# Optimization experiments

Hardware: AMD Instinct MI355X
Metric: run time of the kernel (lower is better)

The kernel has to match this reference:

```python
import jax, jax.numpy as jnp
import numpy as np

B, C, NQ, NK, S, H, FF = 8, 256, 1024, 4096, 16, 8, 2048
DH = C // H
EPS = 1e-5


def _layernorm(x, g, b):
    m = jnp.mean(x, axis=-1, keepdims=True)
    v = jnp.mean((x - m) ** 2, axis=-1, keepdims=True)
    return (x - m) * jax.lax.rsqrt(v + EPS) * g + b


def _box_query(key_pos, query_pos):
    # key_pos: (B,NK,3); query_pos: (B,NQ,6) = centers ++ box sizes (L,H,W)
    centers = query_pos[:, :, None, :3]            # (B,NQ,1,3)
    half = 0.5 * query_pos[:, :, None, 3:]         # (B,NQ,1,3)
    off = jnp.abs(key_pos[:, None, :, :] - centers)  # (B,NQ,NK,3)
    inside = jnp.all(off <= half, axis=-1)         # (B,NQ,NK)
    # first n_sample inside-points in index order (stable sort: inside first)
    order = jnp.argsort(~inside, axis=-1, stable=True)
    idx = order[..., :S]                           # (B,NQ,S)
    valid = jnp.take_along_axis(inside, idx, axis=-1)
    mask = ~valid                                  # True = padded / masked
    idx = jnp.where(mask, 0, idx)
    mask = mask.at[..., 0].set(False)              # matches cuda path: slot 0 never masked
    return idx, mask


def _forward(query, key, query_pos, key_pos,
             q_w, q_b, k_w, k_b, v_w, v_b, o_w, o_b,
             lin1_w, lin1_b, lin2_w, lin2_b,
             n1_g, n1_b, n2_g, n2_b, qpe_w, qpe_b, kpe_w, kpe_b):
    idx, mask = _box_query(key_pos, query_pos)     # (B,NQ,S), (B,NQ,S)
    # gather neighborhoods
    gxyz = jax.vmap(lambda kp, ix: kp[ix])(key_pos, idx)        # (B,NQ,S,3)
    gxyz = gxyz - query_pos[:, :, None, :3]                     # center-relative
    gfeat = jax.vmap(lambda kf, ix: kf[:, ix])(key, idx)        # (B,C,NQ,S)

    BQ = B * NQ
    kfeat = jnp.transpose(gfeat, (0, 2, 3, 1)).reshape(BQ, S, C)   # (BQ,S,C)
    kpe = gxyz.reshape(BQ, S, 3) @ kpe_w.T + kpe_b                 # cross_embed
    qtok = jnp.transpose(query, (0, 2, 1)).reshape(BQ, C)          # (BQ,C)
    qpe = (query_pos @ qpe_w.T + qpe_b).reshape(BQ, C)             # pos_embed

    # multihead cross-attention: 1 query vs S=16 local keys per group
    kv_in = kfeat + kpe
    qh = ((qtok + qpe) @ q_w.T + q_b).reshape(BQ, H, DH)
    kh = (kv_in @ k_w.T + k_b).reshape(BQ, S, H, DH)
    vh = (kv_in @ v_w.T + v_b).reshape(BQ, S, H, DH)
    scores = jnp.einsum('bhd,bshd->bhs', qh, kh) / np.sqrt(DH)    # (BQ,H,S)
    scores = jnp.where(mask.reshape(BQ, 1, S), -1e30, scores)
    attn = jax.nn.softmax(scores, axis=-1)
    ao = jnp.einsum('bhs,bshd->bhd', attn, vh).reshape(BQ, C)
    ao = ao @ o_w.T + o_b

    x = _layernorm(qtok + ao, n1_g, n1_b)                         # post-norm
    ff = jax.nn.relu(x @ lin1_w.T + lin1_b) @ lin2_w.T + lin2_b
    x = _layernorm(x + ff, n2_g, n2_b)
    return jnp.transpose(x.reshape(B, NQ, C), (0, 2, 1))          # (B,C,NQ)


def setup_inputs() -> dict:
    rng = jax.random.key(0)
    ks = jax.random.split(rng, 24)
    s = 0.02
    query = jax.random.normal(ks[0], (B, C, NQ), jnp.float32)
    key = jax.random.normal(ks[1], (B, C, NK), jnp.float32)
    key_pos = jax.random.uniform(ks[2], (B, NK, 3), jnp.float32)
    centers = jax.random.uniform(ks[3], (B, NQ, 3), jnp.float32)
    sizes = jax.random.uniform(ks[4], (B, NQ, 3), jnp.float32, minval=0.1, maxval=0.4)
    query_pos = jnp.concatenate([centers, sizes], axis=-1)
    p = {
        'q_w': jax.random.normal(ks[5], (C, C)) * s, 'q_b': jnp.zeros((C,)),
        'k_w': jax.random.normal(ks[6], (C, C)) * s, 'k_b': jnp.zeros((C,)),
        'v_w': jax.random.normal(ks[7], (C, C)) * s, 'v_b': jnp.zeros((C,)),
        'o_w': jax.random.normal(ks[8], (C, C)) * s, 'o_b': jnp.zeros((C,)),
        'lin1_w': jax.random.normal(ks[9], (FF, C)) * s, 'lin1_b': jnp.zeros((FF,)),
        'lin2_w': jax.random.normal(ks[10], (C, FF)) * s, 'lin2_b': jnp.zeros((C,)),
        'n1_g': jnp.ones((C,)), 'n1_b': jnp.zeros((C,)),
        'n2_g': jnp.ones((C,)), 'n2_b': jnp.zeros((C,)),
        'qpe_w': jax.random.normal(ks[11], (C, 6)) * s, 'qpe_b': jnp.zeros((C,)),
        'kpe_w': jax.random.normal(ks[12], (C, 3)) * s, 'kpe_b': jnp.zeros((C,)),
    }
    return dict(query=query, key=key, query_pos=query_pos, key_pos=key_pos, **p)


def reference(query, key, query_pos, key_pos,
              q_w, q_b, k_w, k_b, v_w, v_b, o_w, o_b,
              lin1_w, lin1_b, lin2_w, lin2_b,
              n1_g, n1_b, n2_g, n2_b, qpe_w, qpe_b, kpe_w, kpe_b):
    return _forward(query, key, query_pos, key_pos,
                    q_w, q_b, k_w, k_b, v_w, v_b, o_w, o_b,
                    lin1_w, lin1_b, lin2_w, lin2_b,
                    n1_g, n1_b, n2_g, n2_b, qpe_w, qpe_b, kpe_w, kpe_b)
```

## Files before the change

### kernel.cpp

```cpp
#include <hip/hip_runtime.h>
#include <cstdint>

#define B_   8
#define C_   256
#define NQ_  1024
#define NK_  4096
#define S_   16
#define H_   8
#define FF_  2048
#define DH_  32
#define BQ_  (B_*NQ_)
#define EPS_ 1e-5f
#define KS_  8

typedef __bf16 bf16x8 __attribute__((ext_vector_type(8)));
typedef __bf16 bf16x4 __attribute__((ext_vector_type(4)));
typedef float  f32x4  __attribute__((ext_vector_type(4)));

struct CvtArgs {
  const float* src[6];
  __bf16* dst[6];
};

__device__ __forceinline__ void gload_lds16(const void* g, void* l) {
  __builtin_amdgcn_global_load_lds(
      (const __attribute__((address_space(1))) void*)g,
      (__attribute__((address_space(3))) void*)l, 16, 0, 0);
}

#define SEGA 2048
#define SEGB 10240
#define SEGC 12288
#define SEGD 13568
#define NPREP 13584

__global__ __launch_bounds__(256) void k_prep(
    const float* __restrict__ query, const float* __restrict__ key,
    const float* __restrict__ query_pos, const float* __restrict__ key_pos,
    const float* __restrict__ qpe_w, const float* __restrict__ qpe_b,
    const float* __restrict__ k_w, const float* __restrict__ k_b,
    const float* __restrict__ v_w, const float* __restrict__ v_b,
    const float* __restrict__ kpe_w, const float* __restrict__ kpe_b,
    CvtArgs ca,
    __bf16* __restrict__ keyTb, __bf16* __restrict__ qtokb,
    __bf16* __restrict__ qinb,
    float4* __restrict__ Pk, float4* __restrict__ Pv,
    int* __restrict__ idxo, int* __restrict__ masko) {
  __shared__ __align__(16) float smem[1248];
  int blk = blockIdx.x, t = threadIdx.x;
  int tx = t & 31, ty = t >> 5;

  if (blk < SEGA) {
    int lane = t & 63;
    int q = blk * 4 + (t >> 6);
    int b = q >> 10;
    const float* kpb = key_pos + (size_t)b * NK_ * 3;
    const float* qp = query_pos + (size_t)q * 6;
    float cx = qp[0], cy = qp[1], cz = qp[2];
    float hx = 0.5f * qp[3], hy = 0.5f * qp[4], hz = 0.5f * qp[5];
    int* iq = idxo + (size_t)q * S_;
    int found = 0;
    for (int ch = 0; ch < NK_ / 64; ch += 4) {
      float dx[4], dy[4], dz[4];
#pragma unroll
      for (int u = 0; u < 4; ++u) {
        int k = (ch + u) * 64 + lane;
        dx[u] = fabsf(kpb[k * 3 + 0] - cx);
        dy[u] = fabsf(kpb[k * 3 + 1] - cy);
        dz[u] = fabsf(kpb[k * 3 + 2] - cz);
      }
#pragma unroll
      for (int u = 0; u < 4; ++u) {
        bool inside = (dx[u] <= hx) && (dy[u] <= hy) && (dz[u] <= hz);
        unsigned long long bal = __ballot(inside);
        if (inside) {
          int slot = found + __popcll(bal & ((1ull << lane) - 1ull));
          if (slot < S_) iq[slot] = (ch + u) * 64 + lane;
        }
        found += __popcll(bal);
      }
      if (found >= S_) break;
    }
    if (found > S_) found = S_;
    if (lane < S_) {
      int m = (lane < found) ? 0 : 1;
      if (lane >= found) iq[lane] = 0;
      if (lane == 0) m = 0;
      masko[(size_t)q * S_ + lane] = m;
    }
  } else if (blk < SEGB) {
    int local = blk - SEGA;
    float (*tt)[33] = (float(*)[33])smem;
    int x = local & 127, y = (local >> 7) & 7, z = local >> 10;
    int j0 = x * 32, i0 = y * 32;
    const float* inz = key + (size_t)z * C_ * NK_;
    __bf16* outz = keyTb + (size_t)z * NK_ * C_;
#pragma unroll
    for (int r = 0; r < 32; r += 8)
      tt[ty + r][tx] = inz[(size_t)(i0 + ty + r) * NK_ + (j0 + tx)];
    __syncthreads();
#pragma unroll
    for (int r = 0; r < 32; r += 8)
      outz[(size_t)(j0 + ty + r) * C_ + (i0 + tx)] = (__bf16)tt[tx][ty + r];
  } else if (blk < SEGC) {
    int local = blk - SEGB;
    float (*tt)[33] = (float(*)[33])smem;
    float (*sqp)[6] = (float(*)[6])(smem + 1056);
    int x = local & 31, y = (local >> 5) & 7, z = local >> 8;
    int nq0 = x * 32, c0 = y * 32;
    const float* inz = query + (size_t)z * C_ * NQ_;
#pragma unroll
    for (int r = 0; r < 32; r += 8)
      tt[ty + r][tx] = inz[(size_t)(c0 + ty + r) * NQ_ + (nq0 + tx)];
    if (t < 192)
      sqp[t / 6][t % 6] = query_pos[((size_t)z * NQ_ + nq0 + t / 6) * 6 + (t % 6)];
    int c = c0 + tx;
    float w0 = qpe_w[c * 6 + 0], w1 = qpe_w[c * 6 + 1], w2 = qpe_w[c * 6 + 2];
    float w3 = qpe_w[c * 6 + 3], w4 = qpe_w[c * 6 + 4], w5 = qpe_w[c * 6 + 5];
    float wb = qpe_b[c];
    __syncthreads();
#pragma unroll
    for (int r = 0; r < 32; r += 8) {
      int nql = ty + r;
      size_t row = (size_t)z * NQ_ + nq0 + nql;
      float v = tt[tx][nql];
      float pe = wb + sqp[nql][0] * w0 + sqp[nql][1] * w1 + sqp[nql][2] * w2 +
                 sqp[nql][3] * w3 + sqp[nql][4] * w4 + sqp[nql][5] * w5;
      qtokb[row * C_ + c] = (__bf16)v;
      qinb[row * C_ + c] = (__bf16)(v + pe);
    }
  } else if (blk < SEGD) {
    int local = blk - SEGC;
    int idx, base;
    if (local < 64)       { idx = 0; base = local; }
    else if (local < 128) { idx = 1; base = local - 64; }
    else if (local < 192) { idx = 2; base = local - 128; }
    else if (local < 256) { idx = 3; base = local - 192; }
    else if (local < 768) { idx = 4; base = local - 256; }
    else                  { idx = 5; base = local - 768; }
    size_t off = (size_t)base * 1024 + t * 4;
    float4 v = *(const float4*)(ca.src[idx] + off);
    __bf16* o = ca.dst[idx] + off;
    o[0] = (__bf16)v.x; o[1] = (__bf16)v.y; o[2] = (__bf16)v.z; o[3] = (__bf16)v.w;
  } else {
    int local = blk - SEGD;
    int bx = local & 7, bv = local >> 3;
    const float* w  = bv ? v_w : k_w;
    const float* wb = bv ? v_b : k_b;
    float4* P = bv ? Pv : Pk;
    float4 (*red)[8] = (float4(*)[8])smem;
    int nl = t >> 3, ks = (t & 7) * 32;
    int n = bx * 32 + nl;
    const float* wr = w + (size_t)n * C_;
    float p0 = 0.f, p1 = 0.f, p2 = 0.f, pb = 0.f;
#pragma unroll
    for (int k = ks; k < ks + 32; ++k) {
      float wv = wr[k];
      p0 += kpe_w[k * 3 + 0] * wv;
      p1 += kpe_w[k * 3 + 1] * wv;
      p2 += kpe_w[k * 3 + 2] * wv;
      pb += kpe_b[k] * wv;
    }
    red[nl][t & 7] = make_float4(p0, p1, p2, pb);
    __syncthreads();
    if (t < 32) {
      float4 s = red[t][0];
#pragma unroll
      for (int j = 1; j < 8; ++j) {
        float4 r = red[t][j];
        s.x += r.x; s.y += r.y; s.z += r.z; s.w += r.w;
      }
      s.w += wb[bx * 32 + t];
      P[bx * 32 + t] = s;
    }
  }
}

template <int BM, int BN, int RELU, int OUT_BF16>
__device__ __forceinline__ void gemm_body(
    const __bf16* __restrict__ A, const __bf16* __restrict__ Wn,
    const float* __restrict__ bias, void* __restrict__ outp,
    int n0, int m0, int N, int K, int kbeg, int kend) {
  constexpr int MI = BM / 32, JN = BN / 32;
  constexpr int AI = BM / 32, BI = BN / 32;
  __shared__ __align__(16) __bf16 As[BM][64];
  __shared__ __align__(16) __bf16 Bs[BN][64];
  int t = threadIdx.x;
  int lane = t & 63, w = t >> 6;
  int lane16 = lane & 15, quad = lane >> 4;
  int wm = (w & 1) * (BM / 2), wn = (w >> 1) * (BN / 2);
  int l3 = lane >> 3;
  int lc = lane & 7;

  f32x4 acc[MI][JN];
#pragma unroll
  for (int i = 0; i < MI; ++i)
#pragma unroll
    for (int j = 0; j < JN; ++j) acc[i][j] = (f32x4){0.f, 0.f, 0.f, 0.f};

  for (int k0 = kbeg; k0 < kend; k0 += 64) {
#pragma unroll
    for (int i = 0; i < AI; ++i) {
      int j = i * 4 + w;
      int row = j * 8 + l3;
      const __bf16* src = A + (size_t)(m0 + row) * K + k0 + ((lc ^ l3) << 3);
      gload_lds16(src, (char*)&As[0][0] + j * 1024);
    }
#pragma unroll
    for (int i = 0; i < BI; ++i) {
      int j = i * 4 + w;
      int row = j * 8 + l3;
      const __bf16* src = Wn + (size_t)(n0 + row) * K + k0 + ((lc ^ l3) << 3);
      gload_lds16(src, (char*)&Bs[0][0] + j * 1024);
    }
    __syncthreads();
#pragma unroll
    for (int kk = 0; kk < 64; kk += 32) {
      bf16x8 af[MI], bfr[JN];
      int qc = (kk >> 3) + quad;
#pragma unroll
      for (int i = 0; i < MI; ++i) {
        int row = wm + i * 16 + lane16;
        int ch = qc ^ (lane16 & 7);
        af[i] = *(const bf16x8*)((const char*)&As[row][0] + ch * 16);
      }
#pragma unroll
      for (int j = 0; j < JN; ++j) {
        int row = wn + j * 16 + lane16;
        int ch = qc ^ (lane16 & 7);
        bfr[j] = *(const bf16x8*)((const char*)&Bs[row][0] + ch * 16);
      }
#pragma unroll
      for (int i = 0; i < MI; ++i)
#pragma unroll
        for (int j = 0; j < JN; ++j)
          acc[i][j] = __builtin_amdgcn_mfma_f32_16x16x32_bf16(af[i], bfr[j], acc[i][j], 0, 0, 0);
    }
    __syncthreads();
  }

#pragma unroll
  for (int j = 0; j < JN; ++j) {
    int col = n0 + wn + j * 16 + lane16;
    float bv = bias ? bias[col] : 0.f;
#pragma unroll
    for (int i = 0; i < MI; ++i) {
#pragma unroll
      for (int r = 0; r < 4; ++r) {
        int row = m0 + wm + i * 16 + quad * 4 + r;
        float v = acc[i][j][r] + bv;
        if (RELU) v = fmaxf(v, 0.f);
        if (OUT_BF16)
          ((__bf16*)outp)[(size_t)row * N + col] = (__bf16)v;
        else
          ((float*)outp)[(size_t)row * N + col] = v;
      }
    }
  }
}

template <int BM, int BN, int RELU, int OUT_BF16>
__global__ __launch_bounds__(256) void k_gemm(
    const __bf16* __restrict__ A, const __bf16* __restrict__ Wn,
    const float* __restrict__ bias, void* __restrict__ outp, int N, int K) {
  gemm_body<BM, BN, RELU, OUT_BF16>(A, Wn, bias, outp,
                                    blockIdx.x * BN, blockIdx.y * BM, N, K, 0, K);
}

__global__ __launch_bounds__(256) void k_gemmsk(
    const __bf16* __restrict__ A, const __bf16* __restrict__ Wn,
    __bf16* __restrict__ partials) {
  int ks = blockIdx.z;
  int kbeg = ks * (FF_ / KS_), kend = kbeg + FF_ / KS_;
  gemm_body<128, 128, 0, 1>(A, Wn, nullptr,
                            partials + (size_t)ks * BQ_ * C_,
                            blockIdx.x * 128, blockIdx.y * 128, C_, FF_, kbeg, kend);
}

__global__ __launch_bounds__(256) void k_gemmsko(
    const __bf16* __restrict__ A, const __bf16* __restrict__ Wn,
    __bf16* __restrict__ partials) {
  int ks = blockIdx.z;
  int kbeg = ks * 128, kend = kbeg + 128;
  gemm_body<128, 64, 0, 1>(A, Wn, nullptr,
                           partials + (size_t)ks * BQ_ * C_,
                           blockIdx.x * 64, blockIdx.y * 128, C_, C_, kbeg, kend);
}

__global__ __launch_bounds__(256) void k_gemm2(
    const __bf16* __restrict__ keyTb, const __bf16* __restrict__ kvwb,
    __bf16* __restrict__ khvbuf,
    const __bf16* __restrict__ qinb, const __bf16* __restrict__ qwb,
    const float* __restrict__ q_b, __bf16* __restrict__ qhb) {
  int blk = blockIdx.x;
  const __bf16 *A, *Wn; const float* bias; __bf16* outp; int n0, m0, N;
  if (blk < 1024) {
    A = keyTb; Wn = kvwb; bias = nullptr; outp = khvbuf;
    n0 = (blk & 3) * 128; m0 = (blk >> 2) * 128; N = 512;
  } else {
    int l = blk - 1024;
    A = qinb; Wn = qwb; bias = q_b; outp = qhb;
    n0 = (l & 1) * 128; m0 = (l >> 1) * 128; N = 256;
  }
  gemm_body<128, 128, 0, 1>(A, Wn, bias, outp, n0, m0, N, 256, 0, 256);
}

__global__ __launch_bounds__(256) void k_attnf(
    const __bf16* __restrict__ khv,
    const float* __restrict__ key_pos,
    const float* __restrict__ query_pos,
    const int* __restrict__ idx,
    const int* __restrict__ maskb,
    const __bf16* __restrict__ qhb,
    const float4* __restrict__ Pk,
    const float4* __restrict__ Pv,
    __bf16* __restrict__ aob) {
  __shared__ __bf16 kvs[S_][520];
  __shared__ float qrow[C_];
  __shared__ float sc[H_][S_];
  __shared__ float pw[H_][S_];
  __shared__ float4 gx4[S_];
  __shared__ float4 pgxs[H_];
  __shared__ float4 qpks[H_];
  __shared__ int srow[S_], smask[S_];
  int bq = blockIdx.x, b = bq >> 10, t = threadIdx.x;

  if (t < S_) {
    int k = idx[(size_t)bq * S_ + t];
    srow[t] = b * NK_ + k;
    smask[t] = maskb[(size_t)bq * S_ + t];
    const float* kpp = key_pos + ((size_t)b * NK_ + k) * 3;
    const float* qp  = query_pos + (size_t)bq * 6;
    gx4[t] = make_float4(kpp[0] - qp[0], kpp[1] - qp[1], kpp[2] - qp[2], 1.f);
  }
  float qv_t = (float)qhb[(size_t)bq * C_ + t];
  qrow[t] = qv_t;
  {
    float4 p = Pk[t];
    p.x *= qv_t; p.y *= qv_t; p.z *= qv_t; p.w *= qv_t;
#pragma unroll
    for (int off = 16; off >= 1; off >>= 1) {
      p.x += __shfl_xor(p.x, off);
      p.y += __shfl_xor(p.y, off);
      p.z += __shfl_xor(p.z, off);
      p.w += __shfl_xor(p.w, off);
    }
    if ((t & 31) == 0) {
      const float s = 0.17677669529663687f;
      qpks[t >> 5] = make_float4(p.x * s, p.y * s, p.z * s, p.w * s);
    }
  }
  __syncthreads();
  {
    int s = t >> 4, c0 = (t & 15) * 32;
    const __bf16* src = khv + (size_t)srow[s] * 512 + c0;
    *(bf16x8*)&kvs[s][c0]      = *(const bf16x8*)&src[0];
    *(bf16x8*)&kvs[s][c0 + 8]  = *(const bf16x8*)&src[8];
    *(bf16x8*)&kvs[s][c0 + 16] = *(const bf16x8*)&src[16];
    *(bf16x8*)&kvs[s][c0 + 24] = *(const bf16x8*)&src[24];
  }
  __syncthreads();
  if (t < H_ * S_) {
    int h = t >> 4, s = t & (S_ - 1);
    float d = 0.f;
#pragma unroll
    for (int c0 = 0; c0 < 32; c0 += 8) {
      bf16x8 xv = *(const bf16x8*)&kvs[s][h * 32 + c0];
#pragma unroll
      for (int j = 0; j < 8; ++j) d += qrow[h * 32 + c0 + j] * (float)xv[j];
    }
    d *= 0.17677669529663687f;
    float4 g = gx4[s];
    float4 pk = qpks[h];
    d += g.x * pk.x + g.y * pk.y + g.z * pk.z + pk.w;
    if (smask[s]) d = -1e30f;
    sc[h][s] = d;
  }
  __syncthreads();
  if (t < H_) {
    float mx = -3.4e38f;
#pragma unroll
    for (int s = 0; s < S_; ++s) mx = fmaxf(mx, sc[t][s]);
    float e[S_], sum = 0.f;
#pragma unroll
    for (int s = 0; s < S_; ++s) { e[s] = expf(sc[t][s] - mx); sum += e[s]; }
    float inv = 1.f / sum;
    float gxx = 0.f, gyy = 0.f, gzz = 0.f;
#pragma unroll
    for (int s = 0; s < S_; ++s) {
      float p = e[s] * inv;
      pw[t][s] = p;
      float4 g = gx4[s];
      gxx += p * g.x; gyy += p * g.y; gzz += p * g.z;
    }
    pgxs[t] = make_float4(gxx, gyy, gzz, 1.f);
  }
  __syncthreads();
  {
    int h = t >> 5;
    float a = 0.f;
#pragma unroll
    for (int s = 0; s < S_; ++s) a += pw[h][s] * (float)kvs[s][256 + t];
    float4 pv = Pv[t];
    float4 g = pgxs[h];
    a += g.x * pv.x + g.y * pv.y + g.z * pv.z + pv.w;
    aob[(size_t)bq * C_ + t] = (__bf16)a;
  }
}

__global__ __launch_bounds__(256) void k_ln1(const __bf16* __restrict__ xa,
                                             const __bf16* __restrict__ op2,
                                             const float* __restrict__ obias,
                                             const float* __restrict__ g,
                                             const float* __restrict__ bb,
                                             __bf16* __restrict__ outb) {
  int wid = (blockIdx.x * 256 + threadIdx.x) >> 6;
  int lane = threadIdx.x & 63;
  bf16x4 va = *(const bf16x4*)&xa[(size_t)wid * C_ + lane * 4];
  float4 ob4 = *(const float4*)(obias + lane * 4);
  bf16x4 p0 = *(const bf16x4*)&op2[(size_t)wid * C_ + lane * 4];
  bf16x4 p1 = *(const bf16x4*)&op2[(size_t)BQ_ * C_ + (size_t)wid * C_ + lane * 4];
  float x0 = (float)va[0] + ob4.x + (float)p0[0] + (float)p1[0];
  float x1 = (float)va[1] + ob4.y + (float)p0[1] + (float)p1[1];
  float x2 = (float)va[2] + ob4.z + (float)p0[2] + (float)p1[2];
  float x3 = (float)va[3] + ob4.w + (float)p0[3] + (float)p1[3];
  float s = x0 + x1 + x2 + x3;
#pragma unroll
  for (int off = 32; off >= 1; off >>= 1) s += __shfl_xor(s, off);
  float mean = s * (1.f / C_);
  float d0 = x0 - mean, d1 = x1 - mean, d2 = x2 - mean, d3 = x3 - mean;
  float v = d0 * d0 + d1 * d1 + d2 * d2 + d3 * d3;
#pragma unroll
  for (int off = 32; off >= 1; off >>= 1) v += __shfl_xor(v, off);
  float inv = 1.f / sqrtf(v * (1.f / C_) + EPS_);
  float4 g4 = *(const float4*)(g + lane * 4);
  float4 b4 = *(const float4*)(bb + lane * 4);
  __bf16* obp = outb + (size_t)wid * C_ + lane * 4;
  obp[0] = (__bf16)(d0 * inv * g4.x + b4.x);
  obp[1] = (__bf16)(d1 * inv * g4.y + b4.y);
  obp[2] = (__bf16)(d2 * inv * g4.z + b4.z);
  obp[3] = (__bf16)(d3 * inv * g4.w + b4.w);
}

__global__ __launch_bounds__(256) void k_lnt(const __bf16* __restrict__ x1b,
                                             const __bf16* __restrict__ ff2p,
                                             const float* __restrict__ l2bias,
                                             const float* __restrict__ g,
                                             const float* __restrict__ bb,
                                             float* __restrict__ out) {
  __shared__ float buf[32][257];
  int z = blockIdx.y, nq0 = blockIdx.x * 32;
  int t = threadIdx.x;
  int w = t >> 6, lane = t & 63;
  float4 g4 = *(const float4*)(g + lane * 4);
  float4 b4 = *(const float4*)(bb + lane * 4);
  float4 l2b = *(const float4*)(l2bias + lane * 4);
#pragma unroll
  for (int rr = 0; rr < 8; ++rr) {
    int row = w * 8 + rr;
    size_t grow = (size_t)z * NQ_ + nq0 + row;
    bf16x4 va = *(const bf16x4*)&x1b[grow * C_ + lane * 4];
    float x0 = (float)va[0] + l2b.x, x1 = (float)va[1] + l2b.y;
    float x2 = (float)va[2] + l2b.z, x3 = (float)va[3] + l2b.w;
#pragma unroll
    for (int ks = 0; ks < KS_; ++ks) {
      bf16x4 p = *(const bf16x4*)&ff2p[((size_t)ks * BQ_ + grow) * C_ + lane * 4];
      x0 += (float)p[0]; x1 += (float)p[1]; x2 += (float)p[2]; x3 += (float)p[3];
    }
    float s = x0 + x1 + x2 + x3;
#pragma unroll
    for (int off = 32; off >= 1; off >>= 1) s += __shfl_xor(s, off);
    float mean = s * (1.f / C_);
    float d0 = x0 - mean, d1 = x1 - mean, d2 = x2 - mean, d3 = x3 - mean;
    float v = d0 * d0 + d1 * d1 + d2 * d2 + d3 * d3;
#pragma unroll
    for (int off = 32; off >= 1; off >>= 1) v += __shfl_xor(v, off);
    float inv = 1.f / sqrtf(v * (1.f / C_) + EPS_);
    buf[row][lane * 4 + 0] = d0 * inv * g4.x + b4.x;
    buf[row][lane * 4 + 1] = d1 * inv * g4.y + b4.y;
    buf[row][lane * 4 + 2] = d2 * inv * g4.z + b4.z;
    buf[row][lane * 4 + 3] = d3 * inv * g4.w + b4.w;
  }
  __syncthreads();
  int tx = t & 31, ty = t >> 5;
#pragma unroll
  for (int ci = 0; ci < 32; ++ci) {
    int c = ci * 8 + ty;
    out[((size_t)z * C_ + c) * NQ_ + nq0 + tx] = buf[tx][c];
  }
}

extern "C" void kernel_launch(void* const* d_in, const int* in_sizes, int n_in,
                              void* d_out, int out_size, void* d_ws, size_t ws_size,
                              hipStream_t stream) {
  const float* query     = (const float*)d_in[0];
  const float* key       = (const float*)d_in[1];
  const float* query_pos = (const float*)d_in[2];
  const float* key_pos   = (const float*)d_in[3];
  const float* q_w = (const float*)d_in[4];  const float* q_b = (const float*)d_in[5];
  const float* k_w = (const float*)d_in[6];  const float* k_b = (const float*)d_in[7];
  const float* v_w = (const float*)d_in[8];  const float* v_b = (const float*)d_in[9];
  const float* o_w = (const float*)d_in[10]; const float* o_b = (const float*)d_in[11];
  const float* lin1_w = (const float*)d_in[12]; const float* lin1_b = (const float*)d_in[13];
  const float* lin2_w = (const float*)d_in[14]; const float* lin2_b = (const float*)d_in[15];
  const float* n1_g = (const float*)d_in[16]; const float* n1_b = (const float*)d_in[17];
  const float* n2_g = (const float*)d_in[18]; const float* n2_b = (const float*)d_in[19];
  const float* qpe_w = (const float*)d_in[20]; const float* qpe_b = (const float*)d_in[21];
  const float* kpe_w = (const float*)d_in[22]; const float* kpe_b = (const float*)d_in[23];
  float* out = (float*)d_out;

  const size_t BQc = (size_t)BQ_ * C_;
  float* w = (float*)d_ws;
  size_t o = 0;
  __bf16* keyTb = (__bf16*)(w + o); o += (size_t)B_ * NK_ * C_ / 2;
  __bf16* qtokb = (__bf16*)(w + o); o += BQc / 2;
  __bf16* op2  = (__bf16*)(w + o); o += BQc;
  __bf16* khvbuf = (__bf16*)(w + o); o += (size_t)B_ * NK_ * 512 / 2;
  __bf16* ff2p = (__bf16*)(w + o); o += BQc * KS_ / 2;
  __bf16* qinb = (__bf16*)(w + o); o += BQc / 2;
  __bf16* qhb  = (__bf16*)(w + o); o += BQc / 2;
  __bf16* aob  = (__bf16*)(w + o); o += BQc / 2;
  __bf16* x1b  = (__bf16*)(w + o); o += BQc / 2;
  __bf16* qwb  = (__bf16*)(w + o); o += (size_t)C_ * C_ / 2;
  __bf16* kvwb = (__bf16*)(w + o); o += (size_t)C_ * C_;
  __bf16* owb  = (__bf16*)(w + o); o += (size_t)C_ * C_ / 2;
  __bf16* l1b  = (__bf16*)(w + o); o += (size_t)C_ * FF_ / 2;
  __bf16* l2b  = (__bf16*)(w + o); o += (size_t)C_ * FF_ / 2;
  float4* Pk   = (float4*)(w + o); o += C_ * 4;
  float4* Pv   = (float4*)(w + o); o += C_ * 4;
  int* idxb  = (int*)(w + o); o += (size_t)BQ_ * S_;
  int* maskb = (int*)(w + o); o += (size_t)BQ_ * S_;
  __bf16* ff1b = khvbuf;

  CvtArgs ca;
  ca.src[0] = q_w; ca.dst[0] = qwb;
  ca.src[1] = k_w; ca.dst[1] = kvwb;
  ca.src[2] = v_w; ca.dst[2] = kvwb + (size_t)C_ * C_;
  ca.src[3] = o_w; ca.dst[3] = owb;
  ca.src[4] = lin1_w; ca.dst[4] = l1b;
  ca.src[5] = lin2_w; ca.dst[5] = l2b;
  k_prep<<<NPREP, 256, 0, stream>>>(query, key, query_pos, key_pos,
                                    qpe_w, qpe_b, k_w, k_b, v_w, v_b,
                                    kpe_w, kpe_b, ca,
                                    keyTb, qtokb, qinb, Pk, Pv, idxb, maskb);
  k_gemm2<<<1024 + 128, 256, 0, stream>>>(keyTb, kvwb, khvbuf, qinb, qwb, q_b, qhb);
  k_attnf<<<BQ_, 256, 0, stream>>>(khvbuf, key_pos, query_pos, idxb, maskb,
                                   qhb, Pk, Pv, aob);
  k_gemmsko<<<dim3(C_ / 64, BQ_ / 128, 2), 256, 0, stream>>>(aob, owb, op2);
  k_ln1<<<BQ_ / 4, 256, 0, stream>>>(qtokb, op2, o_b, n1_g, n1_b, x1b);
  k_gemm<128, 128, 1, 1><<<dim3(FF_ / 128, BQ_ / 128), 256, 0, stream>>>(
      x1b, l1b, lin1_b, ff1b, FF_, C_);
  k_gemmsk<<<dim3(C_ / 128, BQ_ / 128, KS_), 256, 0, stream>>>(ff1b, l2b, ff2p);
  k_lnt<<<dim3(NQ_ / 32, B_), 256, 0, stream>>>(x1b, ff2p, lin2_b, n2_g, n2_b, out);
}
```

Measured before the change: 258.5 us.

## Widen GEMM tiles to 128x256, halve lin2 split-K, drop out-proj split-K

Result: slower. 277.7 us (+7.4%).

```diff
diff --git a/kernel.cpp b/kernel.cpp
--- a/kernel.cpp
+++ b/kernel.cpp
@@ -11,7 +11,7 @@
 #define DH_  32
 #define BQ_  (B_*NQ_)
 #define EPS_ 1e-5f
-#define KS_  8
+#define KS_  4
 
 typedef __bf16 bf16x8 __attribute__((ext_vector_type(8)));
 typedef __bf16 bf16x4 __attribute__((ext_vector_type(4)));
@@ -272,19 +272,9 @@
     __bf16* __restrict__ partials) {
   int ks = blockIdx.z;
   int kbeg = ks * (FF_ / KS_), kend = kbeg + FF_ / KS_;
-  gemm_body<128, 128, 0, 1>(A, Wn, nullptr,
+  gemm_body<128, 256, 0, 1>(A, Wn, nullptr,
                             partials + (size_t)ks * BQ_ * C_,
-                            blockIdx.x * 128, blockIdx.y * 128, C_, FF_, kbeg, kend);
-}
-
-__global__ __launch_bounds__(256) void k_gemmsko(
-    const __bf16* __restrict__ A, const __bf16* __restrict__ Wn,
-    __bf16* __restrict__ partials) {
-  int ks = blockIdx.z;
-  int kbeg = ks * 128, kend = kbeg + 128;
-  gemm_body<128, 64, 0, 1>(A, Wn, nullptr,
-                           partials + (size_t)ks * BQ_ * C_,
-                           blockIdx.x * 64, blockIdx.y * 128, C_, C_, kbeg, kend);
+                            blockIdx.x * 256, blockIdx.y * 128, C_, FF_, kbeg, kend);
 }
 
 __global__ __launch_bounds__(256) void k_gemm2(
@@ -294,15 +284,15 @@
     const float* __restrict__ q_b, __bf16* __restrict__ qhb) {
   int blk = blockIdx.x;
   const __bf16 *A, *Wn; const float* bias; __bf16* outp; int n0, m0, N;
-  if (blk < 1024) {
+  if (blk < 512) {
     A = keyTb; Wn = kvwb; bias = nullptr; outp = khvbuf;
-    n0 = (blk & 3) * 128; m0 = (blk >> 2) * 128; N = 512;
+    n0 = (blk & 1) * 256; m0 = (blk >> 1) * 128; N = 512;
   } else {
-    int l = blk - 1024;
+    int l = blk - 512;
     A = qinb; Wn = qwb; bias = q_b; outp = qhb;
-    n0 = (l & 1) * 128; m0 = (l >> 1) * 128; N = 256;
-  }
-  gemm_body<128, 128, 0, 1>(A, Wn, bias, outp, n0, m0, N, 256, 0, 256);
+    n0 = 0; m0 = l * 128; N = 256;
+  }
+  gemm_body<128, 256, 0, 1>(A, Wn, bias, outp, n0, m0, N, 256, 0, 256);
 }
 
 __global__ __launch_bounds__(256) void k_attnf(
@@ -409,21 +399,18 @@
 }
 
 __global__ __launch_bounds__(256) void k_ln1(const __bf16* __restrict__ xa,
-                                             const __bf16* __restrict__ op2,
-                                             const float* __restrict__ obias,
+                                             const __bf16* __restrict__ op,
                                              const float* __restrict__ g,
                                              const float* __restrict__ bb,
                                              __bf16* __restrict__ outb) {
   int wid = (blockIdx.x * 256 + threadIdx.x) >> 6;
   int lane = threadIdx.x & 63;
   bf16x4 va = *(const bf16x4*)&xa[(size_t)wid * C_ + lane * 4];
-  float4 ob4 = *(const float4*)(obias + lane * 4);
-  bf16x4 p0 = *(const bf16x4*)&op2[(size_t)wid * C_ + lane * 4];
-  bf16x4 p1 = *(const bf16x4*)&op2[(size_t)BQ_ * C_ + (size_t)wid * C_ + lane * 4];
-  float x0 = (float)va[0] + ob4.x + (float)p0[0] + (float)p1[0];
-  float x1 = (float)va[1] + ob4.y + (float)p0[1] + (float)p1[1];
-  float x2 = (float)va[2] + ob4.z + (float)p0[2] + (float)p1[2];
-  float x3 = (float)va[3] + ob4.w + (float)p0[3] + (float)p1[3];
+  bf16x4 p0 = *(const bf16x4*)&op[(size_t)wid * C_ + lane * 4];
+  float x0 = (float)va[0] + (float)p0[0];
+  float x1 = (float)va[1] + (float)p0[1];
+  float x2 = (float)va[2] + (float)p0[2];
+  float x3 = (float)va[3] + (float)p0[3];
   float s = x0 + x1 + x2 + x3;
 #pragma unroll
   for (int off = 32; off >= 1; off >>= 1) s += __shfl_xor(s, off);
@@ -514,7 +501,7 @@
   size_t o = 0;
   __bf16* keyTb = (__bf16*)(w + o); o += (size_t)B_ * NK_ * C_ / 2;
   __bf16* qtokb = (__bf16*)(w + o); o += BQc / 2;
-  __bf16* op2  = (__bf16*)(w + o); o += BQc;
+  __bf16* op   = (__bf16*)(w + o); o += BQc / 2;
   __bf16* khvbuf = (__bf16*)(w + o); o += (size_t)B_ * NK_ * 512 / 2;
   __bf16* ff2p = (__bf16*)(w + o); o += BQc * KS_ / 2;
   __bf16* qinb = (__bf16*)(w + o); o += BQc / 2;
@@ -543,13 +530,14 @@
                                     qpe_w, qpe_b, k_w, k_b, v_w, v_b,
                                     kpe_w, kpe_b, ca,
                                     keyTb, qtokb, qinb, Pk, Pv, idxb, maskb);
-  k_gemm2<<<1024 + 128, 256, 0, stream>>>(keyTb, kvwb, khvbuf, qinb, qwb, q_b, qhb);
+  k_gemm2<<<512 + 64, 256, 0, stream>>>(keyTb, kvwb, khvbuf, qinb, qwb, q_b, qhb);
   k_attnf<<<BQ_, 256, 0, stream>>>(khvbuf, key_pos, query_pos, idxb, maskb,
                                    qhb, Pk, Pv, aob);
-  k_gemmsko<<<dim3(C_ / 64, BQ_ / 128, 2), 256, 0, stream>>>(aob, owb, op2);
-  k_ln1<<<BQ_ / 4, 256, 0, stream>>>(qtokb, op2, o_b, n1_g, n1_b, x1b);
-  k_gemm<128, 128, 1, 1><<<dim3(FF_ / 128, BQ_ / 128), 256, 0, stream>>>(
+  k_gemm<128, 64, 0, 1><<<dim3(C_ / 64, BQ_ / 128), 256, 0, stream>>>(
+      aob, owb, o_b, op, C_, C_);
+  k_ln1<<<BQ_ / 4, 256, 0, stream>>>(qtokb, op, n1_g, n1_b, x1b);
+  k_gemm<128, 256, 1, 1><<<dim3(FF_ / 256, BQ_ / 128), 256, 0, stream>>>(
       x1b, l1b, lin1_b, ff1b, FF_, C_);
-  k_gemmsk<<<dim3(C_ / 128, BQ_ / 128, KS_), 256, 0, stream>>>(ff1b, l2b, ff2p);
+  k_gemmsk<<<dim3(1, BQ_ / 128, KS_), 256, 0, stream>>>(ff1b, l2b, ff2p);
   k_lnt<<<dim3(NQ_ / 32, B_), 256, 0, stream>>>(x1b, ff2p, lin2_b, n2_g, n2_b, out);
 }
```

## Fuse output-proj and FF2 GEMMs with layernorm epilogues, dropping split-K partials

Applied to the files above, without the earlier changes.

Measured after the change: 258.4 us. No clear change (-0.0%).

```diff
diff --git a/kernel.cpp b/kernel.cpp
--- a/kernel.cpp
+++ b/kernel.cpp
@@ -11,7 +11,6 @@
 #define DH_  32
 #define BQ_  (B_*NQ_)
 #define EPS_ 1e-5f
-#define KS_  8
 
 typedef __bf16 bf16x8 __attribute__((ext_vector_type(8)));
 typedef __bf16 bf16x4 __attribute__((ext_vector_type(4)));
@@ -176,21 +175,75 @@
   }
 }
 
+template <int BM, int BN>
+__device__ __forceinline__ void gemm_tile(
+    const __bf16* __restrict__ A, const __bf16* __restrict__ Wn,
+    int m0, int n0, int K, int kbeg, int kend,
+    __bf16 (*As)[64], __bf16 (*Bs)[64],
+    f32x4 (&acc)[BM / 32][BN / 32]) {
+  constexpr int MI = BM / 32, JN = BN / 32;
+  constexpr int AI = BM / 32, BI = BN / 32;
+  int t = threadIdx.x;
+  int lane = t & 63, w = t >> 6;
+  int lane16 = lane & 15, quad = lane >> 4;
+  int wm = (w & 1) * (BM / 2), wn = (w >> 1) * (BN / 2);
+  int l3 = lane >> 3;
+  int lc = lane & 7;
+
+  for (int k0 = kbeg; k0 < kend; k0 += 64) {
+#pragma unroll
+    for (int i = 0; i < AI; ++i) {
+      int j = i * 4 + w;
+      int row = j * 8 + l3;
+      const __bf16* src = A + (size_t)(m0 + row) * K + k0 + ((lc ^ l3) << 3);
+      gload_lds16(src, (char*)&As[0][0] + j * 1024);
+    }
+#pragma unroll
+    for (int i = 0; i < BI; ++i) {
+      int j = i * 4 + w;
+      int row = j * 8 + l3;
+      const __bf16* src = Wn + (size_t)(n0 + row) * K + k0 + ((lc ^ l3) << 3);
+      gload_lds16(src, (char*)&Bs[0][0] + j * 1024);
+    }
+    __syncthreads();
+#pragma unroll
+    for (int kk = 0; kk < 64; kk += 32) {
+      bf16x8 af[MI], bfr[JN];
+      int qc = (kk >> 3) + quad;
+#pragma unroll
+      for (int i = 0; i < MI; ++i) {
+        int row = wm + i * 16 + lane16;
+        int ch = qc ^ (lane16 & 7);
+        af[i] = *(const bf16x8*)((const char*)&As[row][0] + ch * 16);
+      }
+#pragma unroll
+      for (int j = 0; j < JN; ++j) {
+        int row = wn + j * 16 + lane16;
+        int ch = qc ^ (lane16 & 7);
+        bfr[j] = *(const bf16x8*)((const char*)&Bs[row][0] + ch * 16);
+      }
+#pragma unroll
+      for (int i = 0; i < MI; ++i)
+#pragma unroll
+        for (int j = 0; j < JN; ++j)
+          acc[i][j] = __builtin_amdgcn_mfma_f32_16x16x32_bf16(af[i], bfr[j], acc[i][j], 0, 0, 0);
+    }
+    __syncthreads();
+  }
+}
+
 template <int BM, int BN, int RELU, int OUT_BF16>
 __device__ __forceinline__ void gemm_body(
     const __bf16* __restrict__ A, const __bf16* __restrict__ Wn,
     const float* __restrict__ bias, void* __restrict__ outp,
     int n0, int m0, int N, int K, int kbeg, int kend) {
   constexpr int MI = BM / 32, JN = BN / 32;
-  constexpr int AI = BM / 32, BI = BN / 32;
   __shared__ __align__(16) __bf16 As[BM][64];
   __shared__ __align__(16) __bf16 Bs[BN][64];
   int t = threadIdx.x;
   int lane = t & 63, w = t >> 6;
   int lane16 = lane & 15, quad = lane >> 4;
   int wm = (w & 1) * (BM / 2), wn = (w >> 1) * (BN / 2);
-  int l3 = lane >> 3;
-  int lc = lane & 7;
 
   f32x4 acc[MI][JN];
 #pragma unroll
@@ -198,46 +251,7 @@
 #pragma unroll
     for (int j = 0; j < JN; ++j) acc[i][j] = (f32x4){0.f, 0.f, 0.f, 0.f};
 
-  for (int k0 = kbeg; k0 < kend; k0 += 64) {
-#pragma unroll
-    for (int i = 0; i < AI; ++i) {
-      int j = i * 4 + w;
-      int row = j * 8 + l3;
-      const __bf16* src = A + (size_t)(m0 + row) * K + k0 + ((lc ^ l3) << 3);
-      gload_lds16(src, (char*)&As[0][0] + j * 1024);
-    }
-#pragma unroll
-    for (int i = 0; i < BI; ++i) {
-      int j = i * 4 + w;
-      int row = j * 8 + l3;
-      const __bf16* src = Wn + (size_t)(n0 + row) * K + k0 + ((lc ^ l3) << 3);
-      gload_lds16(src, (char*)&Bs[0][0] + j * 1024);
-    }
-    __syncthreads();
-#pragma unroll
-    for (int kk = 0; kk < 64; kk += 32) {
-      bf16x8 af[MI], bfr[JN];
-      int qc = (kk >> 3) + quad;
-#pragma unroll
-      for (int i = 0; i < MI; ++i) {
-        int row = wm + i * 16 + lane16;
-        int ch = qc ^ (lane16 & 7);
-        af[i] = *(const bf16x8*)((const char*)&As[row][0] + ch * 16);
-      }
-#pragma unroll
-      for (int j = 0; j < JN; ++j) {
-        int row = wn + j * 16 + lane16;
-        int ch = qc ^ (lane16 & 7);
-        bfr[j] = *(const bf16x8*)((const char*)&Bs[row][0] + ch * 16);
-      }
-#pragma unroll
-      for (int i = 0; i < MI; ++i)
-#pragma unroll
-        for (int j = 0; j < JN; ++j)
-          acc[i][j] = __builtin_amdgcn_mfma_f32_16x16x32_bf16(af[i], bfr[j], acc[i][j], 0, 0, 0);
-    }
-    __syncthreads();
-  }
+  gemm_tile<BM, BN>(A, Wn, m0, n0, K, kbeg, kend, As, Bs, acc);
 
 #pragma unroll
   for (int j = 0; j < JN; ++j) {
@@ -265,26 +279,6 @@
     const float* __restrict__ bias, void* __restrict__ outp, int N, int K) {
   gemm_body<BM, BN, RELU, OUT_BF16>(A, Wn, bias, outp,
                                     blockIdx.x * BN, blockIdx.y * BM, N, K, 0, K);
-}
-
-__global__ __launch_bounds__(256) void k_gemmsk(
-    const __bf16* __restrict__ A, const __bf16* __restrict__ Wn,
-    __bf16* __restrict__ partials) {
-  int ks = blockIdx.z;
-  int kbeg = ks * (FF_ / KS_), kend = kbeg + FF_ / KS_;
-  gemm_body<128, 128, 0, 1>(A, Wn, nullptr,
-                            partials + (size_t)ks * BQ_ * C_,
-                            blockIdx.x * 128, blockIdx.y * 128, C_, FF_, kbeg, kend);
-}
-
-__global__ __launch_bounds__(256) void k_gemmsko(
-    const __bf16* __restrict__ A, const __bf16* __restrict__ Wn,
-    __bf16* __restrict__ partials) {
-  int ks = blockIdx.z;
-  int kbeg = ks * 128, kend = kbeg + 128;
-  gemm_body<128, 64, 0, 1>(A, Wn, nullptr,
-                           partials + (size_t)ks * BQ_ * C_,
-                           blockIdx.x * 64, blockIdx.y * 128, C_, C_, kbeg, kend);
 }
 
 __global__ __launch_bounds__(256) void k_gemm2(
@@ -303,6 +297,127 @@
     n0 = (l & 1) * 128; m0 = (l >> 1) * 128; N = 256;
   }
   gemm_body<128, 128, 0, 1>(A, Wn, bias, outp, n0, m0, N, 256, 0, 256);
+}
+
+__global__ __launch_bounds__(256) void k_oln(
+    const __bf16* __restrict__ A , const __bf16* __restrict__ Wn ,
+    const float* __restrict__ obias, const __bf16* __restrict__ qtokb,
+    const float* __restrict__ g, const float* __restrict__ bb,
+    __bf16* __restrict__ x1b) {
+  __shared__ __align__(16) __bf16 As[32][64];
+  __shared__ __align__(16) __bf16 Bs[256][64];
+  __shared__ float buf[32][257];
+  int m0 = blockIdx.x * 32;
+  int t = threadIdx.x;
+  int lane = t & 63, w = t >> 6;
+  int lane16 = lane & 15, quad = lane >> 4;
+  int wm = (w & 1) * 16, wn = (w >> 1) * 128;
+
+  f32x4 acc[1][8];
+#pragma unroll
+  for (int j = 0; j < 8; ++j) acc[0][j] = (f32x4){0.f, 0.f, 0.f, 0.f};
+  gemm_tile<32, 256>(A, Wn, m0, 0, C_, 0, C_, As, Bs, acc);
+
+#pragma unroll
+  for (int j = 0; j < 8; ++j) {
+    int col = wn + j * 16 + lane16;
+    float bv = obias[col];
+#pragma unroll
+    for (int r = 0; r < 4; ++r)
+      buf[wm + quad * 4 + r][col] = acc[0][j][r] + bv;
+  }
+  __syncthreads();
+
+#pragma unroll
+  for (int rr = 0; rr < 8; ++rr) {
+    int row = w * 8 + rr;
+    size_t grow = (size_t)(m0 + row);
+    bf16x4 q4 = *(const bf16x4*)&qtokb[grow * C_ + lane * 4];
+    float x0 = buf[row][lane * 4 + 0] + (float)q4[0];
+    float x1 = buf[row][lane * 4 + 1] + (float)q4[1];
+    float x2 = buf[row][lane * 4 + 2] + (float)q4[2];
+    float x3 = buf[row][lane * 4 + 3] + (float)q4[3];
+    float s = x0 + x1 + x2 + x3;
+#pragma unroll
+    for (int off = 32; off >= 1; off >>= 1) s += __shfl_xor(s, off);
+    float mean = s * (1.f / C_);
+    float d0 = x0 - mean, d1 = x1 - mean, d2 = x2 - mean, d3 = x3 - mean;
+    float v = d0 * d0 + d1 * d1 + d2 * d2 + d3 * d3;
+#pragma unroll
+    for (int off = 32; off >= 1; off >>= 1) v += __shfl_xor(v, off);
+    float inv = 1.f / sqrtf(v * (1.f / C_) + EPS_);
+    float4 g4 = *(const float4*)(g + lane * 4);
+    float4 b4 = *(const float4*)(bb + lane * 4);
+    __bf16* obp = x1b + grow * C_ + lane * 4;
+    obp[0] = (__bf16)(d0 * inv * g4.x + b4.x);
+    obp[1] = (__bf16)(d1 * inv * g4.y + b4.y);
+    obp[2] = (__bf16)(d2 * inv * g4.z + b4.z);
+    obp[3] = (__bf16)(d3 * inv * g4.w + b4.w);
+  }
+}
+
+__global__ __launch_bounds__(256) void k_ff2lnt(
+    const __bf16* __restrict__ A , const __bf16* __restrict__ Wn ,
+    const float* __restrict__ l2bias, const __bf16* __restrict__ x1b,
+    const float* __restrict__ g, const float* __restrict__ bb,
+    float* __restrict__ out) {
+  __shared__ __align__(16) __bf16 As[32][64];
+  __shared__ __align__(16) __bf16 Bs[256][64];
+  __shared__ float buf[32][257];
+  int m0 = blockIdx.x * 32;
+  int t = threadIdx.x;
+  int lane = t & 63, w = t >> 6;
+  int lane16 = lane & 15, quad = lane >> 4;
+  int wm = (w & 1) * 16, wn = (w >> 1) * 128;
+
+  f32x4 acc[1][8];
+#pragma unroll
+  for (int j = 0; j < 8; ++j) acc[0][j] = (f32x4){0.f, 0.f, 0.f, 0.f};
+  gemm_tile<32, 256>(A, Wn, m0, 0, FF_, 0, FF_, As, Bs, acc);
+
+#pragma unroll
+  for (int j = 0; j < 8; ++j) {
+    int col = wn + j * 16 + lane16;
+    float bv = l2bias[col];
+#pragma unroll
+    for (int r = 0; r < 4; ++r)
+      buf[wm + quad * 4 + r][col] = acc[0][j][r] + bv;
+  }
+  __syncthreads();
+
+  float4 g4 = *(const float4*)(g + lane * 4);
+  float4 b4 = *(const float4*)(bb + lane * 4);
+#pragma unroll
+  for (int rr = 0; rr < 8; ++rr) {
+    int row = w * 8 + rr;
+    size_t grow = (size_t)(m0 + row);
+    bf16x4 v4 = *(const bf16x4*)&x1b[grow * C_ + lane * 4];
+    float x0 = buf[row][lane * 4 + 0] + (float)v4[0];
+    float x1 = buf[row][lane * 4 + 1] + (float)v4[1];
+    float x2 = buf[row][lane * 4 + 2] + (float)v4[2];
+    float x3 = buf[row][lane * 4 + 3] + (float)v4[3];
+    float s = x0 + x1 + x2 + x3;
+#pragma unroll
+    for (int off = 32; off >= 1; off >>= 1) s += __shfl_xor(s, off);
+    float mean = s * (1.f / C_);
+    float d0 = x0 - mean, d1 = x1 - mean, d2 = x2 - mean, d3 = x3 - mean;
+    float v = d0 * d0 + d1 * d1 + d2 * d2 + d3 * d3;
+#pragma unroll
+    for (int off = 32; off >= 1; off >>= 1) v += __shfl_xor(v, off);
+    float inv = 1.f / sqrtf(v * (1.f / C_) + EPS_);
+    buf[row][lane * 4 + 0] = d0 * inv * g4.x + b4.x;
+    buf[row][lane * 4 + 1] = d1 * inv * g4.y + b4.y;
+    buf[row][lane * 4 + 2] = d2 * inv * g4.z + b4.z;
+    buf[row][lane * 4 + 3] = d3 * inv * g4.w + b4.w;
+  }
+  __syncthreads();
+  int z = m0 >> 10, nq0 = m0 & (NQ_ - 1);
+  int tx = t & 31, ty = t >> 5;
+#pragma unroll
+  for (int ci = 0; ci < 32; ++ci) {
+    int c = ci * 8 + ty;
+    out[((size_t)z * C_ + c) * NQ_ + nq0 + tx] = buf[tx][c];
+  }
 }
 
 __global__ __launch_bounds__(256) void k_attnf(
@@ -408,88 +523,6 @@
   }
 }
 
-__global__ __launch_bounds__(256) void k_ln1(const __bf16* __restrict__ xa,
-                                             const __bf16* __restrict__ op2,
-                                             const float* __restrict__ obias,
-                                             const float* __restrict__ g,
-                                             const float* __restrict__ bb,
-                                             __bf16* __restrict__ outb) {
-  int wid = (blockIdx.x * 256 + threadIdx.x) >> 6;
-  int lane = threadIdx.x & 63;
-  bf16x4 va = *(const bf16x4*)&xa[(size_t)wid * C_ + lane * 4];
-  float4 ob4 = *(const float4*)(obias + lane * 4);
-  bf16x4 p0 = *(const bf16x4*)&op2[(size_t)wid * C_ + lane * 4];
-  bf16x4 p1 = *(const bf16x4*)&op2[(size_t)BQ_ * C_ + (size_t)wid * C_ + lane * 4];
-  float x0 = (float)va[0] + ob4.x + (float)p0[0] + (float)p1[0];
-  float x1 = (float)va[1] + ob4.y + (float)p0[1] + (float)p1[1];
-  float x2 = (float)va[2] + ob4.z + (float)p0[2] + (float)p1[2];
-  float x3 = (float)va[3] + ob4.w + (float)p0[3] + (float)p1[3];
-  float s = x0 + x1 + x2 + x3;
-#pragma unroll
-  for (int off = 32; off >= 1; off >>= 1) s += __shfl_xor(s, off);
-  float mean = s * (1.f / C_);
-  float d0 = x0 - mean, d1 = x1 - mean, d2 = x2 - mean, d3 = x3 - mean;
-  float v = d0 * d0 + d1 * d1 + d2 * d2 + d3 * d3;
-#pragma unroll
-  for (int off = 32; off >= 1; off >>= 1) v += __shfl_xor(v, off);
-  float inv = 1.f / sqrtf(v * (1.f / C_) + EPS_);
-  float4 g4 = *(const float4*)(g + lane * 4);
-  float4 b4 = *(const float4*)(bb + lane * 4);
-  __bf16* obp = outb + (size_t)wid * C_ + lane * 4;
-  obp[0] = (__bf16)(d0 * inv * g4.x + b4.x);
-  obp[1] = (__bf16)(d1 * inv * g4.y + b4.y);
-  obp[2] = (__bf16)(d2 * inv * g4.z + b4.z);
-  obp[3] = (__bf16)(d3 * inv * g4.w + b4.w);
-}
-
-__global__ __launch_bounds__(256) void k_lnt(const __bf16* __restrict__ x1b,
-                                             const __bf16* __restrict__ ff2p,
-                                             const float* __restrict__ l2bias,
-                                             const float* __restrict__ g,
-                                             const float* __restrict__ bb,
-                                             float* __restrict__ out) {
-  __shared__ float buf[32][257];
-  int z = blockIdx.y, nq0 = blockIdx.x * 32;
-  int t = threadIdx.x;
-  int w = t >> 6, lane = t & 63;
-  float4 g4 = *(const float4*)(g + lane * 4);
-  float4 b4 = *(const float4*)(bb + lane * 4);
-  float4 l2b = *(const float4*)(l2bias + lane * 4);
-#pragma unroll
-  for (int rr = 0; rr < 8; ++rr) {
-    int row = w * 8 + rr;
-    size_t grow = (size_t)z * NQ_ + nq0 + row;
-    bf16x4 va = *(const bf16x4*)&x1b[grow * C_ + lane * 4];
-    float x0 = (float)va[0] + l2b.x, x1 = (float)va[1] + l2b.y;
-    float x2 = (float)va[2] + l2b.z, x3 = (float)va[3] + l2b.w;
-#pragma unroll
-    for (int ks = 0; ks < KS_; ++ks) {
-      bf16x4 p = *(const bf16x4*)&ff2p[((size_t)ks * BQ_ + grow) * C_ + lane * 4];
-      x0 += (float)p[0]; x1 += (float)p[1]; x2 += (float)p[2]; x3 += (float)p[3];
-    }
-    float s = x0 + x1 + x2 + x3;
-#pragma unroll
-    for (int off = 32; off >= 1; off >>= 1) s += __shfl_xor(s, off);
-    float mean = s * (1.f / C_);
-    float d0 = x0 - mean, d1 = x1 - mean, d2 = x2 - mean, d3 = x3 - mean;
-    float v = d0 * d0 + d1 * d1 + d2 * d2 + d3 * d3;
-#pragma unroll
-    for (int off = 32; off >= 1; off >>= 1) v += __shfl_xor(v, off);
-    float inv = 1.f / sqrtf(v * (1.f / C_) + EPS_);
-    buf[row][lane * 4 + 0] = d0 * inv * g4.x + b4.x;
-    buf[row][lane * 4 + 1] = d1 * inv * g4.y + b4.y;
-    buf[row][lane * 4 + 2] = d2 * inv * g4.z + b4.z;
-    buf[row][lane * 4 + 3] = d3 * inv * g4.w + b4.w;
-  }
-  __syncthreads();
-  int tx = t & 31, ty = t >> 5;
-#pragma unroll
-  for (int ci = 0; ci < 32; ++ci) {
-    int c = ci * 8 + ty;
-    out[((size_t)z * C_ + c) * NQ_ + nq0 + tx] = buf[tx][c];
-  }
-}
-
 extern "C" void kernel_launch(void* const* d_in, const int* in_sizes, int n_in,
                               void* d_out, int out_size, void* d_ws, size_t ws_size,
                               hipStream_t stream) {
@@ -514,9 +547,7 @@
   size_t o = 0;
   __bf16* keyTb = (__bf16*)(w + o); o += (size_t)B_ * NK_ * C_ / 2;
   __bf16* qtokb = (__bf16*)(w + o); o += BQc / 2;
-  __bf16* op2  = (__bf16*)(w + o); o += BQc;
   __bf16* khvbuf = (__bf16*)(w + o); o += (size_t)B_ * NK_ * 512 / 2;
-  __bf16* ff2p = (__bf16*)(w + o); o += BQc * KS_ / 2;
   __bf16* qinb = (__bf16*)(w + o); o += BQc / 2;
   __bf16* qhb  = (__bf16*)(w + o); o += BQc / 2;
   __bf16* aob  = (__bf16*)(w + o); o += BQc / 2;
@@ -546,10 +577,8 @@
   k_gemm2<<<1024 + 128, 256, 0, stream>>>(keyTb, kvwb, khvbuf, qinb, qwb, q_b, qhb);
   k_attnf<<<BQ_, 256, 0, stream>>>(khvbuf, key_pos, query_pos, idxb, maskb,
                                    qhb, Pk, Pv, aob);
-  k_gemmsko<<<dim3(C_ / 64, BQ_ / 128, 2), 256, 0, stream>>>(aob, owb, op2);
-  k_ln1<<<BQ_ / 4, 256, 0, stream>>>(qtokb, op2, o_b, n1_g, n1_b, x1b);
+  k_oln<<<BQ_ / 32, 256, 0, stream>>>(aob, owb, o_b, qtokb, n1_g, n1_b, x1b);
   k_gemm<128, 128, 1, 1><<<dim3(FF_ / 128, BQ_ / 128), 256, 0, stream>>>(
       x1b, l1b, lin1_b, ff1b, FF_, C_);
-  k_gemmsk<<<dim3(C_ / 128, BQ_ / 128, KS_), 256, 0, stream>>>(ff1b, l2b, ff2p);
-  k_lnt<<<dim3(NQ_ / 32, B_), 256, 0, stream>>>(x1b, ff2p, lin2_b, n2_g, n2_b, out);
-}
+  k_ff2lnt<<<BQ_ / 32, 256, 0, stream>>>(ff1b, l2b, lin2_b, x1b, n2_g, n2_b, out);
+}
```
